# Optimization experiments

Hardware: AMD Instinct MI355X
Metric: run time of the kernel (lower is better)

The kernel has to match this reference:

```python
import jax, jax.numpy as jnp
import numpy as np

AUDIO_DIM, SEM_DIM, ATTN_DIM = 512, 768, 128


def setup_inputs() -> dict:
    key = jax.random.key(0)
    ks = jax.random.split(key, 12)
    B, T, T_sem = 8, 4096, 1024
    s = lambda d: 1.0 / np.sqrt(d)
    return {
        "x_ct": jax.random.normal(ks[0], (B, AUDIO_DIM, T), jnp.float32),
        "sem_btd": jax.random.normal(ks[1], (B, T_sem, SEM_DIM), jnp.float32),
        "ln_w": jnp.ones((AUDIO_DIM,), jnp.float32),
        "ln_b": jnp.zeros((AUDIO_DIM,), jnp.float32),
        "Wq": jax.random.normal(ks[2], (AUDIO_DIM, ATTN_DIM), jnp.float32) * s(AUDIO_DIM),
        "bq": jnp.zeros((ATTN_DIM,), jnp.float32),
        "Wk": jax.random.normal(ks[3], (SEM_DIM, ATTN_DIM), jnp.float32) * s(SEM_DIM),
        "bk": jnp.zeros((ATTN_DIM,), jnp.float32),
        "Wv": jax.random.normal(ks[4], (SEM_DIM, ATTN_DIM), jnp.float32) * s(SEM_DIM),
        "bv": jnp.zeros((ATTN_DIM,), jnp.float32),
        "Wo": jax.random.normal(ks[5], (ATTN_DIM, AUDIO_DIM), jnp.float32) * s(ATTN_DIM),
        "bo": jnp.zeros((AUDIO_DIM,), jnp.float32),
    }


def _layernorm(x, w, b, eps=1e-5):
    mu = jnp.mean(x, axis=-1, keepdims=True)
    var = jnp.mean(jnp.square(x - mu), axis=-1, keepdims=True)
    return (x - mu) * jax.lax.rsqrt(var + eps) * w + b


def reference(x_ct, sem_btd, ln_w, ln_b, Wq, bq, Wk, bk, Wv, bv, Wo, bo):
    # x_ct: [B, C, T] -> [B, T, C]
    x = jnp.swapaxes(x_ct, 1, 2)
    x = _layernorm(x, ln_w, ln_b)
    Q = x @ Wq + bq                      # [B, T, A]
    K = sem_btd @ Wk + bk                # [B, S, A]
    V = sem_btd @ Wv + bv                # [B, S, A]
    scale = ATTN_DIM ** -0.5
    attn = jnp.einsum("bta,bsa->bts", Q, K) * scale
    attn = jax.nn.softmax(attn, axis=-1)  # dropout: eval mode (identity)
    ctx = jnp.einsum("bts,bsa->bta", attn, V)
    delta = ctx @ Wo + bo                # [B, T, C]
    return jnp.swapaxes(delta, 1, 2)     # [B, C, T]
```

## Files before the change

kernel.cpp:

```cpp
#include <hip/hip_runtime.h>
#include <hip/hip_bf16.h>
#include <math.h>

#define BATCH 8
#define TDIM 4096
#define SDIM 1024
#define CDIM 512
#define DDIM 768
#define ADIM 128

typedef short s8v __attribute__((ext_vector_type(8)));
typedef float f4v __attribute__((ext_vector_type(4)));

__device__ __forceinline__ short f2bf(float f) {
    unsigned u = __float_as_uint(f);
    u += 0x7fffu + ((u >> 16) & 1u);
    return (short)(u >> 16);
}

__device__ __forceinline__ f4v mfma16(s8v a, s8v b, f4v c) {
    return __builtin_amdgcn_mfma_f32_16x16x32_bf16(a, b, c, 0, 0, 0);
}

__global__ __launch_bounds__(256) void prep_w(
    const float* __restrict__ Wq, const float* __restrict__ Wk,
    const float* __restrict__ Wv, const float* __restrict__ Wo,
    short* __restrict__ WqT, short* __restrict__ WkT,
    short* __restrict__ WvT, short* __restrict__ WoT)
{
    int gid = blockIdx.x * 256 + threadIdx.x;
    {
        int k = gid >> 7, n = gid & 127;
        WqT[n * 512 + k] = f2bf(Wq[gid]);
    }
    #pragma unroll
    for (int i = 0; i < 2; ++i) {
        int e = gid + i * 65536;
        if (e < 98304) {
            int k = e >> 7, n = e & 127;
            WkT[n * 768 + k] = f2bf(Wk[e]);
            WvT[n * 768 + k] = f2bf(Wv[e]);
        }
    }
    {
        int k = gid >> 9, c = gid & 511;
        WoT[c * 128 + k] = f2bf(Wo[gid]);
    }
}

__global__ __launch_bounds__(256) void kv_proj(
    const float* __restrict__ sem,
    const short* __restrict__ WkT, const float* __restrict__ bk,
    const short* __restrict__ WvT, const float* __restrict__ bv,
    short* __restrict__ Kb, short* __restrict__ Vb)
{
    __shared__ __align__(16) short sA [64 * 40];
    __shared__ __align__(16) short sWk[128 * 40];
    __shared__ __align__(16) short sWv[128 * 40];
    const int tid = threadIdx.x, lane = tid & 63, wave = tid >> 6;
    const int ln15 = lane & 15, q = lane >> 4, kq = q * 8;
    const int r0 = blockIdx.x * 64;
    const int b = r0 >> 10, sbase = r0 & 1023;

    f4v accK[8], accV[8];
    #pragma unroll
    for (int j = 0; j < 8; ++j) { accK[j] = (f4v)0.0f; accV[j] = (f4v)0.0f; }

    const int srow = tid >> 2;
    const int skq  = (tid & 3) * 8;

    for (int kc = 0; kc < DDIM / 32; ++kc) {
        __syncthreads();
        {
            const float* p = sem + (size_t)(r0 + srow) * DDIM + kc * 32 + skq;
            float4 f0 = *(const float4*)p;
            float4 f1 = *(const float4*)(p + 4);
            s8v v;
            v[0]=f2bf(f0.x); v[1]=f2bf(f0.y); v[2]=f2bf(f0.z); v[3]=f2bf(f0.w);
            v[4]=f2bf(f1.x); v[5]=f2bf(f1.y); v[6]=f2bf(f1.z); v[7]=f2bf(f1.w);
            *(s8v*)&sA[srow * 40 + skq] = v;
        }
        #pragma unroll
        for (int i = 0; i < 2; ++i) {
            int idx8 = i * 256 + tid;
            int n = idx8 >> 2, k8 = (idx8 & 3) * 8;
            *(s8v*)&sWk[n * 40 + k8] = *(const s8v*)&WkT[(size_t)n * 768 + kc * 32 + k8];
            *(s8v*)&sWv[n * 40 + k8] = *(const s8v*)&WvT[(size_t)n * 768 + kc * 32 + k8];
        }
        __syncthreads();
        int m = wave * 16 + ln15;
        s8v a = *(const s8v*)&sA[m * 40 + kq];
        #pragma unroll
        for (int j = 0; j < 8; ++j) {
            s8v bK = *(const s8v*)&sWk[(j * 16 + ln15) * 40 + kq];
            accK[j] = mfma16(a, bK, accK[j]);
            s8v bV = *(const s8v*)&sWv[(j * 16 + ln15) * 40 + kq];
            accV[j] = mfma16(a, bV, accV[j]);
        }
    }
    const int s_in_b = sbase + wave * 16 + q * 4;
    #pragma unroll
    for (int j = 0; j < 8; ++j) {
        int col = j * 16 + ln15;
        float biasK = bk[col], biasV = bv[col];
        #pragma unroll
        for (int r = 0; r < 4; ++r)
            Kb[((size_t)b * SDIM + s_in_b + r) * ADIM + col] = f2bf(accK[j][r] + biasK);
        unsigned p0 = (unsigned short)f2bf(accV[j][0] + biasV)
                    | ((unsigned)(unsigned short)f2bf(accV[j][1] + biasV) << 16);
        unsigned p1 = (unsigned short)f2bf(accV[j][2] + biasV)
                    | ((unsigned)(unsigned short)f2bf(accV[j][3] + biasV) << 16);
        uint2 pk; pk.x = p0; pk.y = p1;
        *(uint2*)&Vb[((size_t)b * ADIM + col) * SDIM + s_in_b] = pk;
    }
}

__global__ __launch_bounds__(256) void ln_q(
    const float* __restrict__ x, const float* __restrict__ lnw, const float* __restrict__ lnb,
    const short* __restrict__ WqT, const float* __restrict__ bq, short* __restrict__ Qb)
{
    __shared__ __align__(16) short xt[32 * 520];
    __shared__ __align__(16) short sWq[128 * 72];
    __shared__ float red1[8 * 32], red2[8 * 32];
    __shared__ float smu[32], srs[32];
    const int tid = threadIdx.x, lane = tid & 63, wave = tid >> 6;
    const int ln15 = lane & 15, q = lane >> 4, kq = q * 8;
    const int b = blockIdx.x >> 7;
    const int t0 = (blockIdx.x & 127) * 32;
    const float* xb = x + (size_t)b * CDIM * TDIM;

    {
        int tl = tid & 31, p = tid >> 5;
        float s1 = 0.f, s2 = 0.f;
        const float* pp = xb + (size_t)(p * 64) * TDIM + t0 + tl;
        #pragma unroll 4
        for (int c = 0; c < 64; ++c) { float v = pp[(size_t)c * TDIM]; s1 += v; s2 += v * v; }
        red1[p * 32 + tl] = s1; red2[p * 32 + tl] = s2;
    }
    __syncthreads();
    if (tid < 32) {
        float s1 = 0.f, s2 = 0.f;
        #pragma unroll
        for (int p = 0; p < 8; ++p) { s1 += red1[p * 32 + tid]; s2 += red2[p * 32 + tid]; }
        float mu = s1 * (1.f / 512.f);
        float var = s2 * (1.f / 512.f) - mu * mu;
        smu[tid] = mu; srs[tid] = rsqrtf(var + 1e-5f);
    }
    __syncthreads();
    #pragma unroll
    for (int i = 0; i < 16; ++i) {
        int idx = i * 256 + tid;
        int c = idx >> 3, tq = (idx & 7) * 4;
        float4 f = *(const float4*)&xb[(size_t)c * TDIM + t0 + tq];
        float w = lnw[c], bb_ = lnb[c];
        float vv[4] = { f.x, f.y, f.z, f.w };
        #pragma unroll
        for (int jj = 0; jj < 4; ++jj) {
            int t = tq + jj;
            xt[t * 520 + c] = f2bf((vv[jj] - smu[t]) * srs[t] * w + bb_);
        }
    }
    f4v acc[4];
    #pragma unroll
    for (int j = 0; j < 4; ++j) acc[j] = (f4v)0.0f;
    const int m  = (wave & 1) * 16 + ln15;
    const int jb = (wave >> 1) * 4;
    for (int kc = 0; kc < 8; ++kc) {
        __syncthreads();
        #pragma unroll
        for (int i = 0; i < 4; ++i) {
            int idx8 = i * 256 + tid;
            int n = idx8 >> 3, k8 = (idx8 & 7) * 8;
            *(s8v*)&sWq[n * 72 + k8] = *(const s8v*)&WqT[(size_t)n * 512 + kc * 64 + k8];
        }
        __syncthreads();
        #pragma unroll
        for (int kk = 0; kk < 2; ++kk) {
            s8v a = *(const s8v*)&xt[m * 520 + kc * 64 + kk * 32 + kq];
            #pragma unroll
            for (int j = 0; j < 4; ++j) {
                s8v bb = *(const s8v*)&sWq[((jb + j) * 16 + ln15) * 72 + kk * 32 + kq];
                acc[j] = mfma16(a, bb, acc[j]);
            }
        }
    }
    const float scale = 0.08838834764831845f;
    #pragma unroll
    for (int j = 0; j < 4; ++j) {
        int col = (jb + j) * 16 + ln15;
        float bias = bq[col];
        #pragma unroll
        for (int r = 0; r < 4; ++r) {
            int t = t0 + (wave & 1) * 16 + q * 4 + r;
            Qb[((size_t)b * TDIM + t) * ADIM + col] = f2bf((acc[j][r] + bias) * scale);
        }
    }
}

__global__ __launch_bounds__(256) void attn(
    const short* __restrict__ Qb, const short* __restrict__ Kb,
    const short* __restrict__ Vb, short* __restrict__ Cx)
{
    __shared__ __align__(16) short sQ [64 * 136];
    __shared__ __align__(16) short sK [64 * 136];
    __shared__ __align__(16) short sVT[128 * 72];
    __shared__ __align__(16) short sP [64 * 72];
    const int tid = threadIdx.x, lane = tid & 63, wave = tid >> 6;
    const int ln15 = lane & 15, q = lane >> 4, kq = q * 8;
    const int b = blockIdx.x >> 6;
    const int t0 = (blockIdx.x & 63) * 64;
    const int m = wave * 16 + ln15;

    #pragma unroll
    for (int i = 0; i < 4; ++i) {
        int idx8 = i * 256 + tid;
        int row = idx8 >> 4, a8 = (idx8 & 15) * 8;
        *(s8v*)&sQ[row * 136 + a8] = *(const s8v*)&Qb[((size_t)b * TDIM + t0 + row) * ADIM + a8];
    }
    f4v accO[8];
    #pragma unroll
    for (int j = 0; j < 8; ++j) accO[j] = (f4v)0.0f;
    float lsum[4] = { 0.f, 0.f, 0.f, 0.f };

    for (int sc = 0; sc < SDIM / 64; ++sc) {
        __syncthreads();
        const int s0 = sc * 64;
        #pragma unroll
        for (int i = 0; i < 4; ++i) {
            int idx8 = i * 256 + tid;
            int row = idx8 >> 4, a8 = (idx8 & 15) * 8;
            *(s8v*)&sK[row * 136 + a8] = *(const s8v*)&Kb[((size_t)b * SDIM + s0 + row) * ADIM + a8];
        }
        #pragma unroll
        for (int i = 0; i < 4; ++i) {
            int idx8 = i * 256 + tid;
            int a = idx8 >> 3, s8 = (idx8 & 7) * 8;
            *(s8v*)&sVT[a * 72 + s8] = *(const s8v*)&Vb[((size_t)b * ADIM + a) * SDIM + s0 + s8];
        }
        __syncthreads();
        #pragma unroll
        for (int j = 0; j < 4; ++j) {
            f4v sacc = (f4v)0.0f;
            #pragma unroll
            for (int kc = 0; kc < 4; ++kc) {
                s8v a  = *(const s8v*)&sQ[m * 136 + kc * 32 + kq];
                s8v bb = *(const s8v*)&sK[(j * 16 + ln15) * 136 + kc * 32 + kq];
                sacc = mfma16(a, bb, sacc);
            }
            float ev[4];
            #pragma unroll
            for (int r = 0; r < 4; ++r) {
                ev[r] = __expf(sacc[r]);
                sP[(wave * 16 + q * 4 + r) * 72 + j * 16 + ln15] = f2bf(ev[r]);
            }
            #pragma unroll
            for (int r = 0; r < 4; ++r) {
                float v = ev[r];
                v += __shfl_xor(v, 1);
                v += __shfl_xor(v, 2);
                v += __shfl_xor(v, 4);
                v += __shfl_xor(v, 8);
                lsum[r] += v;
            }
        }
        #pragma unroll
        for (int j = 0; j < 8; ++j) {
            #pragma unroll
            for (int kc = 0; kc < 2; ++kc) {
                s8v a  = *(const s8v*)&sP[m * 72 + kc * 32 + kq];
                s8v bb = *(const s8v*)&sVT[(j * 16 + ln15) * 72 + kc * 32 + kq];
                accO[j] = mfma16(a, bb, accO[j]);
            }
        }
    }
    #pragma unroll
    for (int j = 0; j < 8; ++j) {
        int col = j * 16 + ln15;
        #pragma unroll
        for (int r = 0; r < 4; ++r) {
            int t = t0 + wave * 16 + q * 4 + r;
            Cx[((size_t)b * TDIM + t) * ADIM + col] = f2bf(accO[j][r] / lsum[r]);
        }
    }
}

__global__ __launch_bounds__(256) void out_proj(
    const short* __restrict__ Cx, const short* __restrict__ WoT,
    const float* __restrict__ bo, float* __restrict__ out)
{
    __shared__ __align__(16) short sCtx[64 * 136];
    __shared__ __align__(16) char  buf[128 * 136 * 2];
    short* sWoT = (short*)buf;
    float* outT = (float*)buf;
    const int tid = threadIdx.x, lane = tid & 63, wave = tid >> 6;
    const int ln15 = lane & 15, q = lane >> 4, kq = q * 8;
    const int b = blockIdx.x >> 8;
    const int rem = blockIdx.x & 255;
    const int t0 = (rem & 63) * 64;
    const int c0 = (rem >> 6) * 128;

    #pragma unroll
    for (int i = 0; i < 4; ++i) {
        int idx8 = i * 256 + tid;
        int row = idx8 >> 4, a8 = (idx8 & 15) * 8;
        *(s8v*)&sCtx[row * 136 + a8] = *(const s8v*)&Cx[((size_t)b * TDIM + t0 + row) * ADIM + a8];
    }
    #pragma unroll
    for (int i = 0; i < 8; ++i) {
        int idx8 = i * 256 + tid;
        int n = idx8 >> 4, k8 = (idx8 & 15) * 8;
        *(s8v*)&sWoT[n * 136 + k8] = *(const s8v*)&WoT[(size_t)(c0 + n) * ADIM + k8];
    }
    __syncthreads();
    f4v acc[8];
    #pragma unroll
    for (int j = 0; j < 8; ++j) acc[j] = (f4v)0.0f;
    const int m = wave * 16 + ln15;
    #pragma unroll
    for (int kc = 0; kc < 4; ++kc) {
        s8v a = *(const s8v*)&sCtx[m * 136 + kc * 32 + kq];
        #pragma unroll
        for (int j = 0; j < 8; ++j) {
            s8v bb = *(const s8v*)&sWoT[(j * 16 + ln15) * 136 + kc * 32 + kq];
            acc[j] = mfma16(a, bb, acc[j]);
        }
    }
    __syncthreads();
    #pragma unroll
    for (int j = 0; j < 8; ++j) {
        int cl = j * 16 + ln15;
        float bias = bo[c0 + cl];
        #pragma unroll
        for (int r = 0; r < 4; ++r) {
            int tl = wave * 16 + q * 4 + r;
            outT[cl * 68 + tl] = acc[j][r] + bias;
        }
    }
    __syncthreads();
    #pragma unroll
    for (int i = 0; i < 8; ++i) {
        int idx4 = i * 256 + tid;
        int c = idx4 >> 4, t4 = (idx4 & 15) * 4;
        float4 v = *(const float4*)&outT[c * 68 + t4];
        *(float4*)&out[((size_t)b * CDIM + c0 + c) * TDIM + t0 + t4] = v;
    }
}

extern "C" void kernel_launch(void* const* d_in, const int* in_sizes, int n_in,
                              void* d_out, int out_size, void* d_ws, size_t ws_size,
                              hipStream_t stream) {
    const float* x   = (const float*)d_in[0];
    const float* sem = (const float*)d_in[1];
    const float* lnw = (const float*)d_in[2];
    const float* lnb = (const float*)d_in[3];
    const float* Wq  = (const float*)d_in[4];
    const float* bq  = (const float*)d_in[5];
    const float* Wk  = (const float*)d_in[6];
    const float* bk  = (const float*)d_in[7];
    const float* Wv  = (const float*)d_in[8];
    const float* bv  = (const float*)d_in[9];
    const float* Wo  = (const float*)d_in[10];
    const float* bo  = (const float*)d_in[11];
    float* out = (float*)d_out;

    short* ws  = (short*)d_ws;
    short* Qb  = ws;
    short* Kb  = Qb  + (size_t)BATCH * TDIM * ADIM;
    short* Vb  = Kb  + (size_t)BATCH * SDIM * ADIM;
    short* Cx  = Vb  + (size_t)BATCH * SDIM * ADIM;
    short* WqT = Cx  + (size_t)BATCH * TDIM * ADIM;
    short* WkT = WqT + 128 * 512;
    short* WvT = WkT + 128 * 768;
    short* WoT = WvT + 128 * 768;

    hipLaunchKernelGGL(prep_w,  dim3(256),  dim3(256), 0, stream, Wq, Wk, Wv, Wo, WqT, WkT, WvT, WoT);
    hipLaunchKernelGGL(kv_proj, dim3(128),  dim3(256), 0, stream, sem, WkT, bk, WvT, bv, Kb, Vb);
    hipLaunchKernelGGL(ln_q,    dim3(1024), dim3(256), 0, stream, x, lnw, lnb, WqT, bq, Qb);
    hipLaunchKernelGGL(attn,    dim3(512),  dim3(256), 0, stream, Qb, Kb, Vb, Cx);
    hipLaunchKernelGGL(out_proj,dim3(2048), dim3(256), 0, stream, Cx, WoT, bo, out);
}
```

Baseline: 282.0 us.

## Double-buffer attention K/V, single-pass layernorm, split kv_proj waves by K/V

The attention kernel keeps Q in registers and double-buffers K/V tiles through registers into XOR-swizzled shared memory, so global loads overlap compute and one barrier per step is saved. The row sum is now computed with an MFMA against a ones vector instead of shuffles. ln_q reads x once, stashing bf16 values in a swizzled tile while gathering statistics, then normalizes in place, which removes the second global read. kv_proj uses 32-row blocks with waves split between K and V, doubling the grid. The trade-off is that normalizing from bf16-rounded inputs adds a second rounding step and lowers precision.

Result: faster. 234.9 us (-16.7%).

```diff
diff --git a/kernel.cpp b/kernel.cpp
--- a/kernel.cpp
+++ b/kernel.cpp
@@ -17,7 +17,9 @@
     u += 0x7fffu + ((u >> 16) & 1u);
     return (short)(u >> 16);
 }
-
+__device__ __forceinline__ float bf2f(short s) {
+    return __uint_as_float(((unsigned)(unsigned short)s) << 16);
+}
 __device__ __forceinline__ f4v mfma16(s8v a, s8v b, f4v c) {
     return __builtin_amdgcn_mfma_f32_16x16x32_bf16(a, b, c, 0, 0, 0);
 }
@@ -54,64 +56,67 @@
     const short* __restrict__ WvT, const float* __restrict__ bv,
     short* __restrict__ Kb, short* __restrict__ Vb)
 {
-    __shared__ __align__(16) short sA [64 * 40];
-    __shared__ __align__(16) short sWk[128 * 40];
-    __shared__ __align__(16) short sWv[128 * 40];
+    __shared__ __align__(16) short sA[32 * 40];
+    __shared__ __align__(16) short sW[2][128 * 40];
     const int tid = threadIdx.x, lane = tid & 63, wave = tid >> 6;
     const int ln15 = lane & 15, q = lane >> 4, kq = q * 8;
-    const int r0 = blockIdx.x * 64;
+    const int r0 = blockIdx.x * 32;
     const int b = r0 >> 10, sbase = r0 & 1023;
-
-    f4v accK[8], accV[8];
-    #pragma unroll
-    for (int j = 0; j < 8; ++j) { accK[j] = (f4v)0.0f; accV[j] = (f4v)0.0f; }
-
-    const int srow = tid >> 2;
-    const int skq  = (tid & 3) * 8;
+    const int kv = wave >> 1;
+    const int mh = wave & 1;
+    const int m  = mh * 16 + ln15;
+
+    f4v acc[8];
+    #pragma unroll
+    for (int j = 0; j < 8; ++j) acc[j] = (f4v)0.0f;
+
+    const int srow = tid >> 3;
+    const int sk4  = (tid & 7) * 4;
 
     for (int kc = 0; kc < DDIM / 32; ++kc) {
         __syncthreads();
         {
-            const float* p = sem + (size_t)(r0 + srow) * DDIM + kc * 32 + skq;
-            float4 f0 = *(const float4*)p;
-            float4 f1 = *(const float4*)(p + 4);
-            s8v v;
-            v[0]=f2bf(f0.x); v[1]=f2bf(f0.y); v[2]=f2bf(f0.z); v[3]=f2bf(f0.w);
-            v[4]=f2bf(f1.x); v[5]=f2bf(f1.y); v[6]=f2bf(f1.z); v[7]=f2bf(f1.w);
-            *(s8v*)&sA[srow * 40 + skq] = v;
+            float4 f = *(const float4*)&sem[(size_t)(r0 + srow) * DDIM + kc * 32 + sk4];
+            uint2 pk;
+            pk.x = (unsigned short)f2bf(f.x) | ((unsigned)(unsigned short)f2bf(f.y) << 16);
+            pk.y = (unsigned short)f2bf(f.z) | ((unsigned)(unsigned short)f2bf(f.w) << 16);
+            *(uint2*)&sA[srow * 40 + sk4] = pk;
         }
         #pragma unroll
         for (int i = 0; i < 2; ++i) {
             int idx8 = i * 256 + tid;
             int n = idx8 >> 2, k8 = (idx8 & 3) * 8;
-            *(s8v*)&sWk[n * 40 + k8] = *(const s8v*)&WkT[(size_t)n * 768 + kc * 32 + k8];
-            *(s8v*)&sWv[n * 40 + k8] = *(const s8v*)&WvT[(size_t)n * 768 + kc * 32 + k8];
+            *(s8v*)&sW[0][n * 40 + k8] = *(const s8v*)&WkT[(size_t)n * 768 + kc * 32 + k8];
+            *(s8v*)&sW[1][n * 40 + k8] = *(const s8v*)&WvT[(size_t)n * 768 + kc * 32 + k8];
         }
         __syncthreads();
-        int m = wave * 16 + ln15;
         s8v a = *(const s8v*)&sA[m * 40 + kq];
         #pragma unroll
         for (int j = 0; j < 8; ++j) {
-            s8v bK = *(const s8v*)&sWk[(j * 16 + ln15) * 40 + kq];
-            accK[j] = mfma16(a, bK, accK[j]);
-            s8v bV = *(const s8v*)&sWv[(j * 16 + ln15) * 40 + kq];
-            accV[j] = mfma16(a, bV, accV[j]);
-        }
-    }
-    const int s_in_b = sbase + wave * 16 + q * 4;
-    #pragma unroll
-    for (int j = 0; j < 8; ++j) {
-        int col = j * 16 + ln15;
-        float biasK = bk[col], biasV = bv[col];
-        #pragma unroll
-        for (int r = 0; r < 4; ++r)
-            Kb[((size_t)b * SDIM + s_in_b + r) * ADIM + col] = f2bf(accK[j][r] + biasK);
-        unsigned p0 = (unsigned short)f2bf(accV[j][0] + biasV)
-                    | ((unsigned)(unsigned short)f2bf(accV[j][1] + biasV) << 16);
-        unsigned p1 = (unsigned short)f2bf(accV[j][2] + biasV)
-                    | ((unsigned)(unsigned short)f2bf(accV[j][3] + biasV) << 16);
-        uint2 pk; pk.x = p0; pk.y = p1;
-        *(uint2*)&Vb[((size_t)b * ADIM + col) * SDIM + s_in_b] = pk;
+            s8v bb = *(const s8v*)&sW[kv][(j * 16 + ln15) * 40 + kq];
+            acc[j] = mfma16(a, bb, acc[j]);
+        }
+    }
+    const int s_in_b = sbase + mh * 16 + q * 4;
+    if (kv == 0) {
+        #pragma unroll
+        for (int j = 0; j < 8; ++j) {
+            int col = j * 16 + ln15;
+            float bias = bk[col];
+            #pragma unroll
+            for (int r = 0; r < 4; ++r)
+                Kb[((size_t)b * SDIM + s_in_b + r) * ADIM + col] = f2bf(acc[j][r] + bias);
+        }
+    } else {
+        #pragma unroll
+        for (int j = 0; j < 8; ++j) {
+            int col = j * 16 + ln15;
+            float bias = bv[col];
+            uint2 pk;
+            pk.x = (unsigned short)f2bf(acc[j][0] + bias) | ((unsigned)(unsigned short)f2bf(acc[j][1] + bias) << 16);
+            pk.y = (unsigned short)f2bf(acc[j][2] + bias) | ((unsigned)(unsigned short)f2bf(acc[j][3] + bias) << 16);
+            *(uint2*)&Vb[((size_t)b * ADIM + col) * SDIM + s_in_b] = pk;
+        }
     }
 }
 
@@ -119,51 +124,71 @@
     const float* __restrict__ x, const float* __restrict__ lnw, const float* __restrict__ lnb,
     const short* __restrict__ WqT, const float* __restrict__ bq, short* __restrict__ Qb)
 {
-    __shared__ __align__(16) short xt[32 * 520];
-    __shared__ __align__(16) short sWq[128 * 72];
-    __shared__ float red1[8 * 32], red2[8 * 32];
+    __shared__ __align__(16) short xt[32 * 512];
+    __shared__ __align__(16) char  ubuf[128 * 72 * 2];
     __shared__ float smu[32], srs[32];
+    short* sWq  = (short*)ubuf;
+    float* red1 = (float*)ubuf;
+    float* red2 = (float*)(ubuf + 4224);
     const int tid = threadIdx.x, lane = tid & 63, wave = tid >> 6;
     const int ln15 = lane & 15, q = lane >> 4, kq = q * 8;
     const int b = blockIdx.x >> 7;
     const int t0 = (blockIdx.x & 127) * 32;
     const float* xb = x + (size_t)b * CDIM * TDIM;
 
-    {
-        int tl = tid & 31, p = tid >> 5;
-        float s1 = 0.f, s2 = 0.f;
-        const float* pp = xb + (size_t)(p * 64) * TDIM + t0 + tl;
-        #pragma unroll 4
-        for (int c = 0; c < 64; ++c) { float v = pp[(size_t)c * TDIM]; s1 += v; s2 += v * v; }
-        red1[p * 32 + tl] = s1; red2[p * 32 + tl] = s2;
+    const int tq = (tid & 7) * 4;
+    const int g  = tid >> 3;
+    float ps1[4] = {0.f,0.f,0.f,0.f}, ps2[4] = {0.f,0.f,0.f,0.f};
+    #pragma unroll
+    for (int i = 0; i < 16; ++i) {
+        int c = i * 32 + g;
+        float4 f = *(const float4*)&xb[(size_t)c * TDIM + t0 + tq];
+        float vv[4] = { f.x, f.y, f.z, f.w };
+        int kb = c >> 3, cl = c & 7;
+        #pragma unroll
+        for (int jj = 0; jj < 4; ++jj) {
+            int t = tq + jj;
+            ps1[jj] += vv[jj]; ps2[jj] += vv[jj] * vv[jj];
+            xt[t * 512 + ((kb ^ ((t >> 2) & 7)) * 8) + cl] = f2bf(vv[jj]);
+        }
+    }
+    #pragma unroll
+    for (int jj = 0; jj < 4; ++jj) {
+        red1[(tq + jj) * 33 + g] = ps1[jj];
+        red2[(tq + jj) * 33 + g] = ps2[jj];
     }
     __syncthreads();
     if (tid < 32) {
         float s1 = 0.f, s2 = 0.f;
-        #pragma unroll
-        for (int p = 0; p < 8; ++p) { s1 += red1[p * 32 + tid]; s2 += red2[p * 32 + tid]; }
+        #pragma unroll 8
+        for (int gg = 0; gg < 32; ++gg) { s1 += red1[tid * 33 + gg]; s2 += red2[tid * 33 + gg]; }
         float mu = s1 * (1.f / 512.f);
         float var = s2 * (1.f / 512.f) - mu * mu;
         smu[tid] = mu; srs[tid] = rsqrtf(var + 1e-5f);
     }
     __syncthreads();
-    #pragma unroll
-    for (int i = 0; i < 16; ++i) {
-        int idx = i * 256 + tid;
-        int c = idx >> 3, tq = (idx & 7) * 4;
-        float4 f = *(const float4*)&xb[(size_t)c * TDIM + t0 + tq];
-        float w = lnw[c], bb_ = lnb[c];
-        float vv[4] = { f.x, f.y, f.z, f.w };
-        #pragma unroll
-        for (int jj = 0; jj < 4; ++jj) {
-            int t = tq + jj;
-            xt[t * 520 + c] = f2bf((vv[jj] - smu[t]) * srs[t] * w + bb_);
+    {
+        const int cb = tid & 63;
+        const int c8 = cb * 8;
+        float w8[8], b8[8];
+        #pragma unroll
+        for (int jj = 0; jj < 8; ++jj) { w8[jj] = lnw[c8 + jj]; b8[jj] = lnb[c8 + jj]; }
+        #pragma unroll
+        for (int i = 0; i < 8; ++i) {
+            int t = i * 4 + (tid >> 6);
+            float mu = smu[t], rs = srs[t];
+            short* p = &xt[t * 512 + ((cb ^ ((t >> 2) & 7)) * 8)];
+            s8v v = *(s8v*)p;
+            #pragma unroll
+            for (int jj = 0; jj < 8; ++jj)
+                v[jj] = f2bf((bf2f(v[jj]) - mu) * rs * w8[jj] + b8[jj]);
+            *(s8v*)p = v;
         }
     }
     f4v acc[4];
     #pragma unroll
     for (int j = 0; j < 4; ++j) acc[j] = (f4v)0.0f;
-    const int m  = (wave & 1) * 16 + ln15;
+    const int mrow = (wave & 1) * 16 + ln15;
     const int jb = (wave >> 1) * 4;
     for (int kc = 0; kc < 8; ++kc) {
         __syncthreads();
@@ -176,7 +201,8 @@
         __syncthreads();
         #pragma unroll
         for (int kk = 0; kk < 2; ++kk) {
-            s8v a = *(const s8v*)&xt[m * 520 + kc * 64 + kk * 32 + kq];
+            int kb = kc * 8 + kk * 4 + q;
+            s8v a = *(const s8v*)&xt[mrow * 512 + ((kb ^ ((mrow >> 2) & 7)) * 8)];
             #pragma unroll
             for (int j = 0; j < 4; ++j) {
                 s8v bb = *(const s8v*)&sWq[((jb + j) * 16 + ln15) * 72 + kk * 32 + kq];
@@ -201,85 +227,107 @@
     const short* __restrict__ Qb, const short* __restrict__ Kb,
     const short* __restrict__ Vb, short* __restrict__ Cx)
 {
-    __shared__ __align__(16) short sQ [64 * 136];
-    __shared__ __align__(16) short sK [64 * 136];
-    __shared__ __align__(16) short sVT[128 * 72];
-    __shared__ __align__(16) short sP [64 * 72];
+    __shared__ __align__(16) short sK [2][64 * 128];
+    __shared__ __align__(16) short sVT[2][128 * 64];
+    __shared__ __align__(16) short sP [64 * 64];
     const int tid = threadIdx.x, lane = tid & 63, wave = tid >> 6;
     const int ln15 = lane & 15, q = lane >> 4, kq = q * 8;
     const int b = blockIdx.x >> 6;
     const int t0 = (blockIdx.x & 63) * 64;
     const int m = wave * 16 + ln15;
 
+    const int krow = tid >> 4, kkb = tid & 15;
+    const int varow = tid >> 3, vkb = tid & 7;
+
+    s8v qf[4];
+    {
+        const short* qp = Qb + ((size_t)b * TDIM + t0 + m) * ADIM + kq;
+        #pragma unroll
+        for (int kc = 0; kc < 4; ++kc) qf[kc] = *(const s8v*)(qp + kc * 32);
+    }
+    s8v ones;
+    #pragma unroll
+    for (int j = 0; j < 8; ++j) ones[j] = (short)0x3F80;
+
+    f4v accO[8]; f4v accL = (f4v)0.0f;
+    #pragma unroll
+    for (int j = 0; j < 8; ++j) accO[j] = (f4v)0.0f;
+
+    const short* Kbase = Kb + (size_t)b * SDIM * ADIM;
+    const short* Vbase = Vb + (size_t)b * ADIM * SDIM;
+    s8v rk[4], rv[4];
+
     #pragma unroll
     for (int i = 0; i < 4; ++i) {
-        int idx8 = i * 256 + tid;
-        int row = idx8 >> 4, a8 = (idx8 & 15) * 8;
-        *(s8v*)&sQ[row * 136 + a8] = *(const s8v*)&Qb[((size_t)b * TDIM + t0 + row) * ADIM + a8];
-    }
-    f4v accO[8];
-    #pragma unroll
-    for (int j = 0; j < 8; ++j) accO[j] = (f4v)0.0f;
-    float lsum[4] = { 0.f, 0.f, 0.f, 0.f };
+        rk[i] = *(const s8v*)(Kbase + (size_t)(i * 16 + krow) * ADIM + kkb * 8);
+        rv[i] = *(const s8v*)(Vbase + (size_t)(i * 32 + varow) * SDIM + vkb * 8);
+    }
+    #pragma unroll
+    for (int i = 0; i < 4; ++i) {
+        int r = i * 16 + krow;
+        *(s8v*)&sK[0][r * 128 + ((kkb ^ (r & 15)) * 8)] = rk[i];
+        int a = i * 32 + varow;
+        *(s8v*)&sVT[0][a * 64 + ((vkb ^ (a & 7)) * 8)] = rv[i];
+    }
+    __syncthreads();
 
     for (int sc = 0; sc < SDIM / 64; ++sc) {
-        __syncthreads();
-        const int s0 = sc * 64;
-        #pragma unroll
-        for (int i = 0; i < 4; ++i) {
-            int idx8 = i * 256 + tid;
-            int row = idx8 >> 4, a8 = (idx8 & 15) * 8;
-            *(s8v*)&sK[row * 136 + a8] = *(const s8v*)&Kb[((size_t)b * SDIM + s0 + row) * ADIM + a8];
-        }
-        #pragma unroll
-        for (int i = 0; i < 4; ++i) {
-            int idx8 = i * 256 + tid;
-            int a = idx8 >> 3, s8 = (idx8 & 7) * 8;
-            *(s8v*)&sVT[a * 72 + s8] = *(const s8v*)&Vb[((size_t)b * ADIM + a) * SDIM + s0 + s8];
-        }
-        __syncthreads();
+        const int cur = sc & 1;
+        if (sc < 15) {
+            const int s0n = (sc + 1) * 64;
+            #pragma unroll
+            for (int i = 0; i < 4; ++i) {
+                rk[i] = *(const s8v*)(Kbase + (size_t)(s0n + i * 16 + krow) * ADIM + kkb * 8);
+                rv[i] = *(const s8v*)(Vbase + (size_t)(i * 32 + varow) * SDIM + s0n + vkb * 8);
+            }
+        }
         #pragma unroll
         for (int j = 0; j < 4; ++j) {
             f4v sacc = (f4v)0.0f;
+            const int row = j * 16 + ln15;
             #pragma unroll
             for (int kc = 0; kc < 4; ++kc) {
-                s8v a  = *(const s8v*)&sQ[m * 136 + kc * 32 + kq];
-                s8v bb = *(const s8v*)&sK[(j * 16 + ln15) * 136 + kc * 32 + kq];
-                sacc = mfma16(a, bb, sacc);
-            }
-            float ev[4];
+                s8v bb = *(const s8v*)&sK[cur][row * 128 + (((kc * 4 + q) ^ (row & 15)) * 8)];
+                sacc = mfma16(qf[kc], bb, sacc);
+            }
             #pragma unroll
             for (int r = 0; r < 4; ++r) {
-                ev[r] = __expf(sacc[r]);
-                sP[(wave * 16 + q * 4 + r) * 72 + j * 16 + ln15] = f2bf(ev[r]);
-            }
-            #pragma unroll
-            for (int r = 0; r < 4; ++r) {
-                float v = ev[r];
-                v += __shfl_xor(v, 1);
-                v += __shfl_xor(v, 2);
-                v += __shfl_xor(v, 4);
-                v += __shfl_xor(v, 8);
-                lsum[r] += v;
-            }
-        }
+                float ev = __expf(sacc[r]);
+                int prow = wave * 16 + q * 4 + r;
+                int pcol = j * 16 + ln15;
+                sP[prow * 64 + (((pcol >> 3) ^ (prow & 7)) * 8) + (pcol & 7)] = f2bf(ev);
+            }
+        }
+        #pragma unroll
+        for (int kc = 0; kc < 2; ++kc) {
+            s8v pa = *(const s8v*)&sP[m * 64 + (((kc * 4 + q) ^ (m & 7)) * 8)];
+            accL = mfma16(pa, ones, accL);
+            #pragma unroll
+            for (int j = 0; j < 8; ++j) {
+                int a = j * 16 + ln15;
+                s8v bb = *(const s8v*)&sVT[cur][a * 64 + (((kc * 4 + q) ^ (a & 7)) * 8)];
+                accO[j] = mfma16(pa, bb, accO[j]);
+            }
+        }
+        if (sc < 15) {
+            #pragma unroll
+            for (int i = 0; i < 4; ++i) {
+                int r = i * 16 + krow;
+                *(s8v*)&sK[cur ^ 1][r * 128 + ((kkb ^ (r & 15)) * 8)] = rk[i];
+                int a = i * 32 + varow;
+                *(s8v*)&sVT[cur ^ 1][a * 64 + ((vkb ^ (a & 7)) * 8)] = rv[i];
+            }
+        }
+        __syncthreads();
+    }
+    #pragma unroll
+    for (int r = 0; r < 4; ++r) {
+        float rinv = 1.0f / accL[r];
+        int t = t0 + wave * 16 + q * 4 + r;
         #pragma unroll
         for (int j = 0; j < 8; ++j) {
-            #pragma unroll
-            for (int kc = 0; kc < 2; ++kc) {
-                s8v a  = *(const s8v*)&sP[m * 72 + kc * 32 + kq];
-                s8v bb = *(const s8v*)&sVT[(j * 16 + ln15) * 72 + kc * 32 + kq];
-                accO[j] = mfma16(a, bb, accO[j]);
-            }
-        }
-    }
-    #pragma unroll
-    for (int j = 0; j < 8; ++j) {
-        int col = j * 16 + ln15;
-        #pragma unroll
-        for (int r = 0; r < 4; ++r) {
-            int t = t0 + wave * 16 + q * 4 + r;
-            Cx[((size_t)b * TDIM + t) * ADIM + col] = f2bf(accO[j][r] / lsum[r]);
+            int col = j * 16 + ln15;
+            Cx[((size_t)b * TDIM + t) * ADIM + col] = f2bf(accO[j][r] * rinv);
         }
     }
 }
@@ -374,7 +422,7 @@
     short* WoT = WvT + 128 * 768;
 
     hipLaunchKernelGGL(prep_w,  dim3(256),  dim3(256), 0, stream, Wq, Wk, Wv, Wo, WqT, WkT, WvT, WoT);
-    hipLaunchKernelGGL(kv_proj, dim3(128),  dim3(256), 0, stream, sem, WkT, bk, WvT, bv, Kb, Vb);
+    hipLaunchKernelGGL(kv_proj, dim3(256),  dim3(256), 0, stream, sem, WkT, bk, WvT, bv, Kb, Vb);
     hipLaunchKernelGGL(ln_q,    dim3(1024), dim3(256), 0, stream, x, lnw, lnb, WqT, bq, Qb);
     hipLaunchKernelGGL(attn,    dim3(512),  dim3(256), 0, stream, Qb, Kb, Vb, Cx);
     hipLaunchKernelGGL(out_proj,dim3(2048), dim3(256), 0, stream, Cx, WoT, bo, out);
```
